# Kernel tuning notes

Measured on AMD Instinct MI355X. Metric: run time of the kernel, lower is better.

Reference implementation:

```python
import jax, jax.numpy as jnp
import numpy as np

D = 512; NH = 8; DH = D // NH; NL = 4; NQ = 4; CB = 1024; DATA = 256
LN_EPS = 1e-5


def _ln(x, s, b):
    m = jnp.mean(x, -1, keepdims=True)
    v = jnp.var(x, -1, keepdims=True)
    return (x - m) / jnp.sqrt(v + LN_EPS) * s + b


def _pos_embed(T, d):
    pos = jnp.arange(T, dtype=jnp.float32)[:, None]
    div = jnp.exp(jnp.arange(0, d, 2, dtype=jnp.float32) * (-np.log(10000.0) / d))
    pe = jnp.zeros((T, d), jnp.float32)
    pe = pe.at[:, 0::2].set(jnp.sin(pos * div))
    pe = pe.at[:, 1::2].set(jnp.cos(pos * div))
    return pe


def _rotate_to(x, q):
    # rotation trick: reflect x through Householder planes so it aligns with q,
    # gradients flow through x only (rotation itself is stop-gradient)
    eps = 1e-6
    nx = jnp.linalg.norm(x, axis=-1, keepdims=True)
    nq = jnp.linalg.norm(q, axis=-1, keepdims=True)
    u = x / jnp.maximum(nx, eps)
    qn = q / jnp.maximum(nq, eps)
    w = u + qn
    w = jax.lax.stop_gradient(w / jnp.maximum(jnp.linalg.norm(w, axis=-1, keepdims=True), eps))
    u_sg = jax.lax.stop_gradient(u)
    qn_sg = jax.lax.stop_gradient(qn)
    out = x - 2.0 * jnp.sum(x * w, -1, keepdims=True) * w \
            + 2.0 * jnp.sum(x * u_sg, -1, keepdims=True) * qn_sg
    return out * jax.lax.stop_gradient(nq / jnp.maximum(nx, eps))


def _vqvae(x, w_in, b_in, qkv_w, qkv_b, out_w, out_b, ln1_s, ln1_b, ln2_s, ln2_b,
           ff1_w, ff1_b, ff2_w, ff2_b, codebooks,
           dec_ln_s, dec_ln_b, dec_w1, dec_b1, dec_w2, dec_b2):
    B, T, _ = x.shape
    h = x @ w_in + b_in + _pos_embed(T, D)[None]
    causal = jnp.triu(jnp.ones((T, T), dtype=bool), k=1)
    scale = 1.0 / np.sqrt(DH)
    for l in range(NL):
        qkv = h @ qkv_w[l] + qkv_b[l]
        q, k, v = jnp.split(qkv, 3, axis=-1)
        q = q.reshape(B, T, NH, DH).transpose(0, 2, 1, 3)
        k = k.reshape(B, T, NH, DH).transpose(0, 2, 1, 3)
        v = v.reshape(B, T, NH, DH).transpose(0, 2, 1, 3)
        scores = jnp.einsum('bhqd,bhkd->bhqk', q, k) * scale
        scores = jnp.where(causal[None, None], -jnp.inf, scores)
        attn = jax.nn.softmax(scores, axis=-1)
        o = jnp.einsum('bhqk,bhkd->bhqd', attn, v).transpose(0, 2, 1, 3).reshape(B, T, D)
        h = _ln(h + o @ out_w[l] + out_b[l], ln1_s[l], ln1_b[l])
        ff = jax.nn.relu(h @ ff1_w[l] + ff1_b[l]) @ ff2_w[l] + ff2_b[l]
        h = _ln(h + ff, ln2_s[l], ln2_b[l])
    # residual VQ with 4 quantizers, rotation trick, commitment loss
    residual = h
    quant_out = jnp.zeros_like(h)
    idx_list, loss_list = [], []
    for qi in range(NQ):
        cb = codebooks[qi]  # [CB, D]
        d = (jnp.sum(residual ** 2, -1, keepdims=True)
             - 2.0 * residual @ cb.T
             + jnp.sum(cb ** 2, -1)[None, None])  # [B,T,CB]
        idx = jnp.argmin(d, axis=-1)
        qv = cb[idx]
        loss_list.append(0.25 * jnp.mean((jax.lax.stop_gradient(qv) - residual) ** 2))
        quant = _rotate_to(residual, qv)
        residual = residual - jax.lax.stop_gradient(quant)
        quant_out = quant_out + quant
        idx_list.append(idx)
    commit = jnp.stack(loss_list)          # [NQ]
    indices = jnp.stack(idx_list, axis=-1)  # [B,T,NQ]
    dh = _ln(quant_out, dec_ln_s, dec_ln_b)
    dec = jax.nn.gelu(dh @ dec_w1 + dec_b1, approximate=False) @ dec_w2 + dec_b2
    return dec, jnp.mean(commit), indices


def setup_inputs() -> dict:
    key = jax.random.key(0)
    ks = jax.random.split(key, 16)
    B, T = 32, 512
    s = 0.02
    return {
        'x': jax.random.normal(ks[0], (B, T, DATA), jnp.float32),
        'w_in': jax.random.normal(ks[1], (DATA, D), jnp.float32) * s,
        'b_in': jnp.zeros((D,), jnp.float32),
        'qkv_w': jax.random.normal(ks[2], (NL, D, 3 * D), jnp.float32) * s,
        'qkv_b': jnp.zeros((NL, 3 * D), jnp.float32),
        'out_w': jax.random.normal(ks[3], (NL, D, D), jnp.float32) * s,
        'out_b': jnp.zeros((NL, D), jnp.float32),
        'ln1_s': jnp.ones((NL, D), jnp.float32),
        'ln1_b': jnp.zeros((NL, D), jnp.float32),
        'ln2_s': jnp.ones((NL, D), jnp.float32),
        'ln2_b': jnp.zeros((NL, D), jnp.float32),
        'ff1_w': jax.random.normal(ks[4], (NL, D, 4 * D), jnp.float32) * s,
        'ff1_b': jnp.zeros((NL, 4 * D), jnp.float32),
        'ff2_w': jax.random.normal(ks[5], (NL, 4 * D, D), jnp.float32) * s,
        'ff2_b': jnp.zeros((NL, D), jnp.float32),
        'codebooks': jax.random.normal(ks[6], (NQ, CB, D), jnp.float32),
        'dec_ln_s': jnp.ones((D,), jnp.float32),
        'dec_ln_b': jnp.zeros((D,), jnp.float32),
        'dec_w1': jax.random.normal(ks[7], (D, D), jnp.float32) * s,
        'dec_b1': jnp.zeros((D,), jnp.float32),
        'dec_w2': jax.random.normal(ks[8], (D, DATA), jnp.float32) * s,
        'dec_b2': jnp.zeros((DATA,), jnp.float32),
    }


def reference(x, w_in, b_in, qkv_w, qkv_b, out_w, out_b, ln1_s, ln1_b, ln2_s, ln2_b,
              ff1_w, ff1_b, ff2_w, ff2_b, codebooks,
              dec_ln_s, dec_ln_b, dec_w1, dec_b1, dec_w2, dec_b2):
    return _vqvae(x, w_in, b_in, qkv_w, qkv_b, out_w, out_b, ln1_s, ln1_b, ln2_s, ln2_b,
                  ff1_w, ff1_b, ff2_w, ff2_b, codebooks,
                  dec_ln_s, dec_ln_b, dec_w1, dec_b1, dec_w2, dec_b2)
```

## Files before the change

kernel.cpp:

```cpp
#include <hip/hip_runtime.h>
#include <hip/hip_bf16.h>
#include <math.h>

#define DD   512
#define NHH  8
#define DHH  64
#define NLL  4
#define NQQ  4
#define CBB  1024
#define DATA 256
#define BB   32
#define TT   512
#define MM   (BB*TT)

typedef __attribute__((ext_vector_type(8))) short bf16x8;
typedef __attribute__((ext_vector_type(4))) float f32x4;

__device__ __forceinline__ float blk_reduce(float v, float* red) {
    const int t = threadIdx.x;
    red[t] = v;
    __syncthreads();
    #pragma unroll
    for (int s = 128; s > 0; s >>= 1) {
        if (t < s) red[t] += red[t + s];
        __syncthreads();
    }
    float r = red[0];
    __syncthreads();
    return r;
}

__device__ __forceinline__ int xcd_remap_lin(int orig, int nwg) {
    int xcd = orig & 7;
    int q = nwg >> 3, r = nwg & 7;
    int base = (xcd < r) ? xcd * (q + 1) : r * (q + 1) + (xcd - r) * q;
    return base + (orig >> 3);
}

__global__ __launch_bounds__(256) void pe_k(float* __restrict__ pe) {
    int t = blockIdx.x;
    int i = threadIdx.x;
    float dv  = expf((float)(2 * i) * -0.017988946039015984f);
    float arg = (float)t * dv;
    pe[(size_t)t * DD + 2 * i]     = sinf(arg);
    pe[(size_t)t * DD + 2 * i + 1] = cosf(arg);
}

__device__ __forceinline__ void cvt3x8(const float* v, bf16x8& q0, bf16x8& q1, bf16x8& q2) {
    #pragma unroll
    for (int j = 0; j < 8; ++j) {
        float f = v[j];
        unsigned short h0 = (unsigned short)((__float_as_uint(f) + 0x8000u) >> 16);
        float f0 = __uint_as_float((unsigned)h0 << 16);
        float r1 = f - f0;
        unsigned short h1 = (unsigned short)((__float_as_uint(r1) + 0x8000u) >> 16);
        float f1 = __uint_as_float((unsigned)h1 << 16);
        float r2 = r1 - f1;
        unsigned short h2 = (unsigned short)((__float_as_uint(r2) + 0x8000u) >> 16);
        q0[j] = (short)h0; q1[j] = (short)h1; q2[j] = (short)h2;
    }
}
__device__ __forceinline__ void cvt3s(float f, short& h0, short& h1, short& h2) {
    unsigned short a0 = (unsigned short)((__float_as_uint(f) + 0x8000u) >> 16);
    float f0 = __uint_as_float((unsigned)a0 << 16);
    float r1 = f - f0;
    unsigned short a1 = (unsigned short)((__float_as_uint(r1) + 0x8000u) >> 16);
    float f1 = __uint_as_float((unsigned)a1 << 16);
    float r2 = r1 - f1;
    unsigned short a2 = (unsigned short)((__float_as_uint(r2) + 0x8000u) >> 16);
    h0 = (short)a0; h1 = (short)a1; h2 = (short)a2;
}

__device__ __forceinline__ void gld_lds16(const short* src, short* lds) {
    __builtin_amdgcn_global_load_lds(
        (const __attribute__((address_space(1))) unsigned int*)src,
        (__attribute__((address_space(3))) unsigned int*)lds,
        16, 0, 0);
}

__global__ __launch_bounds__(256)
void wsplit_tr_k(const float* __restrict__ W, short* __restrict__ P, int N, int K)
{
    const size_t NK = (size_t)N * K;
    const int n = blockIdx.x * 64 + (threadIdx.x & 63);
    #pragma unroll
    for (int it = 0; it < 2; ++it) {
        int k = blockIdx.y * 64 + ((threadIdx.x >> 6) + it * 4) * 8;
        float v[8];
        #pragma unroll
        for (int j = 0; j < 8; ++j) v[j] = W[(size_t)(k + j) * N + n];
        bf16x8 q0, q1, q2;
        cvt3x8(v, q0, q1, q2);
        size_t o = (size_t)n * K + k;
        *(bf16x8*)&P[o] = q0;
        *(bf16x8*)&P[NK + o] = q1;
        *(bf16x8*)&P[2 * NK + o] = q2;
    }
}
__global__ __launch_bounds__(256)
void wsplit_dir_k(const float* __restrict__ W, short* __restrict__ P, int K, size_t NK)
{
    size_t t = (size_t)blockIdx.x * 256 + threadIdx.x;
    size_t n = t >> 6;
    int k = (int)(t & 63) * 8;
    float v[8];
    *(float4*)&v[0] = *(const float4*)(W + n * K + k);
    *(float4*)&v[4] = *(const float4*)(W + n * K + k + 4);
    bf16x8 q0, q1, q2;
    cvt3x8(v, q0, q1, q2);
    size_t o = n * K + k;
    *(bf16x8*)&P[o] = q0;
    *(bf16x8*)&P[NK + o] = q1;
    *(bf16x8*)&P[2 * NK + o] = q2;
}

enum { EPI_BIAS = 0, EPI_RES = 1, EPI_RELU = 2, EPI_GELU = 3, EPI_PE = 4, EPI_PLAIN = 5 };

template<int EPI>
__global__ __launch_bounds__(256, 3)
void mgemm2_k(const float* __restrict__ A, const short* __restrict__ Bp,
              const float* __restrict__ bias, const float* __restrict__ extra,
              float* __restrict__ Cv, int Mdim, int Ndim, int Kdim)
{
    __shared__ short Bs[3 * 128 * 32];
    const size_t NK = (size_t)Ndim * Kdim;
    const int tid = threadIdx.x;
    const int l   = tid & 63;
    const int w   = tid >> 6;

    int lin = xcd_remap_lin(blockIdx.y * gridDim.x + blockIdx.x, gridDim.x * gridDim.y);
    const int bxx = lin % gridDim.x;
    const int byy = lin / gridDim.x;

    const int wm0 = byy * 128 + w * 32;
    const int bn0 = bxx * 128;
    const int lr  = l & 15;
    const int lk  = (l >> 4) * 8;

    int sp[6], sn[6], sk[6];
    #pragma unroll
    for (int i = 0; i < 6; ++i) {
        int f = i * 4096 + tid * 16;
        sp[i] = f >> 13;
        int r = f & 8191;
        sn[i] = r >> 6;
        sk[i] = ((r & 63) >> 1) ^ (((sn[i] >> 1) & 3) << 3);
    }

    f32x4 acc[2][8];
    #pragma unroll
    for (int i = 0; i < 2; ++i)
        #pragma unroll
        for (int j = 0; j < 8; ++j)
            acc[i][j] = (f32x4){0.f, 0.f, 0.f, 0.f};

    for (int k0 = 0; k0 < Kdim; k0 += 32) {
        __syncthreads();
        #pragma unroll
        for (int i = 0; i < 6; ++i) {
            const short* src = Bp + (size_t)sp[i] * NK + (size_t)(bn0 + sn[i]) * Kdim + k0 + sk[i];
            gld_lds16(src, (short*)((char*)Bs + i * 4096 + w * 1024));
        }

        bf16x8 a0[2], a1[2], a2[2];
        #pragma unroll
        for (int mf = 0; mf < 2; ++mf) {
            const float* p = A + (size_t)(wm0 + mf * 16 + lr) * Kdim + k0 + lk;
            float v[8];
            *(float4*)&v[0] = *(const float4*)p;
            *(float4*)&v[4] = *(const float4*)(p + 4);
            cvt3x8(v, a0[mf], a1[mf], a2[mf]);
        }
        __syncthreads();

        #pragma unroll
        for (int nf = 0; nf < 8; ++nf) {
            int brow = nf * 16 + lr;
            int lkx = lk ^ (((brow >> 1) & 3) << 3);
            bf16x8 b0 = *(const bf16x8*)&Bs[0 * 4096 + brow * 32 + lkx];
            bf16x8 b1 = *(const bf16x8*)&Bs[1 * 4096 + brow * 32 + lkx];
            bf16x8 b2 = *(const bf16x8*)&Bs[2 * 4096 + brow * 32 + lkx];
            #pragma unroll
            for (int mf = 0; mf < 2; ++mf) {
                f32x4 c = acc[mf][nf];
                c = __builtin_amdgcn_mfma_f32_16x16x32_bf16(a0[mf], b0, c, 0, 0, 0);
                c = __builtin_amdgcn_mfma_f32_16x16x32_bf16(a0[mf], b1, c, 0, 0, 0);
                c = __builtin_amdgcn_mfma_f32_16x16x32_bf16(a1[mf], b0, c, 0, 0, 0);
                c = __builtin_amdgcn_mfma_f32_16x16x32_bf16(a1[mf], b1, c, 0, 0, 0);
                c = __builtin_amdgcn_mfma_f32_16x16x32_bf16(a0[mf], b2, c, 0, 0, 0);
                c = __builtin_amdgcn_mfma_f32_16x16x32_bf16(a2[mf], b0, c, 0, 0, 0);
                acc[mf][nf] = c;
            }
        }
    }

    #pragma unroll
    for (int mf = 0; mf < 2; ++mf) {
        #pragma unroll
        for (int r = 0; r < 4; ++r) {
            int m = wm0 + mf * 16 + (l >> 4) * 4 + r;
            #pragma unroll
            for (int nf = 0; nf < 8; ++nf) {
                int n = bn0 + nf * 16 + lr;
                float v = acc[mf][nf][r];
                if constexpr (EPI != EPI_PLAIN) v += bias[n];
                if constexpr (EPI == EPI_RES)  v += extra[(size_t)m * Ndim + n];
                if constexpr (EPI == EPI_PE)   v += extra[(size_t)(m & (TT - 1)) * DD + n];
                if constexpr (EPI == EPI_RELU) v = fmaxf(v, 0.0f);
                if constexpr (EPI == EPI_GELU) v = 0.5f * v * (1.0f + erff(v * 0.70710678118654752f));
                Cv[(size_t)m * Ndim + n] = v;
            }
        }
    }
}

__global__ __launch_bounds__(256, 3)
void distmin2_k(const float* __restrict__ A, const short* __restrict__ Bp,
                const float* __restrict__ cn2,
                float* __restrict__ pval, int* __restrict__ pidx)
{
    __shared__ short Bs[3 * 128 * 32];
    const int Ndim = CBB, Kdim = DD;
    const size_t NK = (size_t)Ndim * Kdim;
    const int tid = threadIdx.x;
    const int l   = tid & 63;
    const int w   = tid >> 6;

    int lin = xcd_remap_lin(blockIdx.y * gridDim.x + blockIdx.x, gridDim.x * gridDim.y);
    const int bxx = lin % gridDim.x;
    const int byy = lin / gridDim.x;

    const int wm0 = byy * 128 + w * 32;
    const int bn0 = bxx * 128;
    const int lr  = l & 15;
    const int lk  = (l >> 4) * 8;

    int sp[6], sn[6], sk[6];
    #pragma unroll
    for (int i = 0; i < 6; ++i) {
        int f = i * 4096 + tid * 16;
        sp[i] = f >> 13;
        int r = f & 8191;
        sn[i] = r >> 6;
        sk[i] = ((r & 63) >> 1) ^ (((sn[i] >> 1) & 3) << 3);
    }

    f32x4 acc[2][8];
    #pragma unroll
    for (int i = 0; i < 2; ++i)
        #pragma unroll
        for (int j = 0; j < 8; ++j)
            acc[i][j] = (f32x4){0.f, 0.f, 0.f, 0.f};

    for (int k0 = 0; k0 < Kdim; k0 += 32) {
        __syncthreads();
        #pragma unroll
        for (int i = 0; i < 6; ++i) {
            const short* src = Bp + (size_t)sp[i] * NK + (size_t)(bn0 + sn[i]) * Kdim + k0 + sk[i];
            gld_lds16(src, (short*)((char*)Bs + i * 4096 + w * 1024));
        }

        bf16x8 a0[2], a1[2], a2[2];
        #pragma unroll
        for (int mf = 0; mf < 2; ++mf) {
            const float* p = A + (size_t)(wm0 + mf * 16 + lr) * Kdim + k0 + lk;
            float v[8];
            *(float4*)&v[0] = *(const float4*)p;
            *(float4*)&v[4] = *(const float4*)(p + 4);
            cvt3x8(v, a0[mf], a1[mf], a2[mf]);
        }
        __syncthreads();

        #pragma unroll
        for (int nf = 0; nf < 8; ++nf) {
            int brow = nf * 16 + lr;
            int lkx = lk ^ (((brow >> 1) & 3) << 3);
            bf16x8 b0 = *(const bf16x8*)&Bs[0 * 4096 + brow * 32 + lkx];
            bf16x8 b1 = *(const bf16x8*)&Bs[1 * 4096 + brow * 32 + lkx];
            bf16x8 b2 = *(const bf16x8*)&Bs[2 * 4096 + brow * 32 + lkx];
            #pragma unroll
            for (int mf = 0; mf < 2; ++mf) {
                f32x4 c = acc[mf][nf];
                c = __builtin_amdgcn_mfma_f32_16x16x32_bf16(a0[mf], b0, c, 0, 0, 0);
                c = __builtin_amdgcn_mfma_f32_16x16x32_bf16(a0[mf], b1, c, 0, 0, 0);
                c = __builtin_amdgcn_mfma_f32_16x16x32_bf16(a1[mf], b0, c, 0, 0, 0);
                c = __builtin_amdgcn_mfma_f32_16x16x32_bf16(a1[mf], b1, c, 0, 0, 0);
                c = __builtin_amdgcn_mfma_f32_16x16x32_bf16(a0[mf], b2, c, 0, 0, 0);
                c = __builtin_amdgcn_mfma_f32_16x16x32_bf16(a2[mf], b0, c, 0, 0, 0);
                acc[mf][nf] = c;
            }
        }
    }

    #pragma unroll
    for (int mf = 0; mf < 2; ++mf) {
        #pragma unroll
        for (int r = 0; r < 4; ++r) {
            int m = wm0 + mf * 16 + (l >> 4) * 4 + r;
            float best = INFINITY; int bi = 0x7fffffff;
            #pragma unroll
            for (int nf = 0; nf < 8; ++nf) {
                int n = bn0 + nf * 16 + lr;
                float d = cn2[n] - 2.0f * acc[mf][nf][r];
                if (d < best) { best = d; bi = n; }
            }
            #pragma unroll
            for (int off = 1; off < 16; off <<= 1) {
                float ov = __shfl_xor(best, off);
                int   oi = __shfl_xor(bi, off);
                if (ov < best || (ov == best && oi < bi)) { best = ov; bi = oi; }
            }
            if (lr == 0) {
                pval[(size_t)m * 8 + bxx] = best;
                pidx[(size_t)m * 8 + bxx] = bi;
            }
        }
    }
}

__global__ __launch_bounds__(256)
void argmin8_k(const float* __restrict__ pval, const int* __restrict__ pidx,
               int* __restrict__ idx)
{
    int row = blockIdx.x * 256 + threadIdx.x;
    float best = INFINITY; int bi = 0x7fffffff;
    #pragma unroll
    for (int j = 0; j < 8; ++j) {
        float v = pval[(size_t)row * 8 + j];
        int  ii = pidx[(size_t)row * 8 + j];
        if (v < best || (v == best && ii < bi)) { best = v; bi = ii; }
    }
    idx[row] = bi;
}

__global__ __launch_bounds__(256, 2)
void mattn_k(const float* __restrict__ qkv, float* __restrict__ o)
{
    const int bid = xcd_remap_lin(blockIdx.x, gridDim.x);
    const int qt = bid & 7;
    const int hh = (bid >> 3) & 7;
    const int bb = bid >> 6;
    const int tid = threadIdx.x;
    const int w  = tid >> 6;
    const int l  = tid & 63;
    const int lr = l & 15;
    const int lg = l >> 4;
    const int lk = lg * 8;

    __shared__ short Kb[3][4096];
    __shared__ short Vb[3][4096];
    __shared__ float Ps[4][1024];

    const float* qbase = qkv + (size_t)bb * TT * 1536 + hh * 64;
    const float* kbase = qbase + DD;
    const float* vbase = qbase + 2 * DD;

    bf16x8 qa[2][3];
    {
        int qrow = qt * 64 + w * 16 + lr;
        #pragma unroll
        for (int dc = 0; dc < 2; ++dc) {
            float v[8];
            const float* p = qbase + (size_t)qrow * 1536 + dc * 32 + lk;
            *(float4*)&v[0] = *(const float4*)p;
            *(float4*)&v[4] = *(const float4*)(p + 4);
            cvt3x8(v, qa[dc][0], qa[dc][1], qa[dc][2]);
        }
    }

    f32x4 oacc[4];
    #pragma unroll
    for (int nf = 0; nf < 4; ++nf) oacc[nf] = (f32x4){0.f, 0.f, 0.f, 0.f};
    float m[4], s[4];
    #pragma unroll
    for (int r = 0; r < 4; ++r) { m[r] = -INFINITY; s[r] = 0.f; }

    for (int kt = 0; kt <= qt; ++kt) {
        __syncthreads();
        {
            int kr = tid >> 2, dseg = (tid & 3) * 16;
            const float* p = kbase + (size_t)(kt * 64 + kr) * 1536 + dseg;
            float v[16];
            *(float4*)&v[0]  = *(const float4*)p;
            *(float4*)&v[4]  = *(const float4*)(p + 4);
            *(float4*)&v[8]  = *(const float4*)(p + 8);
            *(float4*)&v[12] = *(const float4*)(p + 12);
            bf16x8 t0, t1, t2, u0, u1, u2;
            cvt3x8(v, t0, t1, t2);
            cvt3x8(v + 8, u0, u1, u2);
            int si = (kr * 64 + dseg) ^ ((kr & 7) << 3);
            *(bf16x8*)&Kb[0][si] = t0; *(bf16x8*)&Kb[0][si ^ 8] = u0;
            *(bf16x8*)&Kb[1][si] = t1; *(bf16x8*)&Kb[1][si ^ 8] = u1;
            *(bf16x8*)&Kb[2][si] = t2; *(bf16x8*)&Kb[2][si ^ 8] = u2;
        }
        {
            int d = tid & 63, kg = (tid >> 6) * 16;
            const float* p = vbase + (size_t)(kt * 64 + kg) * 1536 + d;
            bf16x8 w0[2], w1[2], w2[2];
            #pragma unroll
            for (int i = 0; i < 16; ++i) {
                float f = p[(size_t)i * 1536];
                short h0, h1, h2; cvt3s(f, h0, h1, h2);
                w0[i >> 3][i & 7] = h0; w1[i >> 3][i & 7] = h1; w2[i >> 3][i & 7] = h2;
            }
            int si = (d * 64 + kg) ^ ((d & 7) << 3);
            *(bf16x8*)&Vb[0][si] = w0[0]; *(bf16x8*)&Vb[0][si ^ 8] = w0[1];
            *(bf16x8*)&Vb[1][si] = w1[0]; *(bf16x8*)&Vb[1][si ^ 8] = w1[1];
            *(bf16x8*)&Vb[2][si] = w2[0]; *(bf16x8*)&Vb[2][si ^ 8] = w2[1];
        }
        __syncthreads();

        f32x4 S4[4];
        #pragma unroll
        for (int nf = 0; nf < 4; ++nf) {
            f32x4 acc = (f32x4){0.f, 0.f, 0.f, 0.f};
            int kcol = nf * 16 + lr;
            int rowx = kcol * 64, sw = (kcol & 7) << 3;
            #pragma unroll
            for (int dc = 0; dc < 2; ++dc) {
                int si = rowx + ((dc * 32 + lk) ^ sw);
                bf16x8 b0 = *(const bf16x8*)&Kb[0][si];
                bf16x8 b1 = *(const bf16x8*)&Kb[1][si];
                bf16x8 b2 = *(const bf16x8*)&Kb[2][si];
                acc = __builtin_amdgcn_mfma_f32_16x16x32_bf16(qa[dc][0], b0, acc, 0, 0, 0);
                acc = __builtin_amdgcn_mfma_f32_16x16x32_bf16(qa[dc][0], b1, acc, 0, 0, 0);
                acc = __builtin_amdgcn_mfma_f32_16x16x32_bf16(qa[dc][1], b0, acc, 0, 0, 0);
                acc = __builtin_amdgcn_mfma_f32_16x16x32_bf16(qa[dc][1], b1, acc, 0, 0, 0);
                acc = __builtin_amdgcn_mfma_f32_16x16x32_bf16(qa[dc][0], b2, acc, 0, 0, 0);
                acc = __builtin_amdgcn_mfma_f32_16x16x32_bf16(qa[dc][2], b0, acc, 0, 0, 0);
            }
            S4[nf] = acc;
        }
        #pragma unroll
        for (int nf = 0; nf < 4; ++nf)
            #pragma unroll
            for (int r = 0; r < 4; ++r) S4[nf][r] *= 0.125f;
        if (kt == qt) {
            #pragma unroll
            for (int nf = 0; nf < 4; ++nf) {
                int kg_ = nf * 16 + lr;
                #pragma unroll
                for (int r = 0; r < 4; ++r) {
                    int qg_ = w * 16 + lg * 4 + r;
                    if (kg_ > qg_) S4[nf][r] = -INFINITY;
                }
            }
        }
        float mnew[4], scl[4], psum[4];
        #pragma unroll
        for (int r = 0; r < 4; ++r) {
            float v = fmaxf(fmaxf(S4[0][r], S4[1][r]), fmaxf(S4[2][r], S4[3][r]));
            v = fmaxf(v, __shfl_xor(v, 1));
            v = fmaxf(v, __shfl_xor(v, 2));
            v = fmaxf(v, __shfl_xor(v, 4));
            v = fmaxf(v, __shfl_xor(v, 8));
            mnew[r] = fmaxf(m[r], v);
            scl[r] = expf(m[r] - mnew[r]);
            psum[r] = 0.f;
        }
        #pragma unroll
        for (int nf = 0; nf < 4; ++nf) {
            #pragma unroll
            for (int r = 0; r < 4; ++r) {
                float p = expf(S4[nf][r] - mnew[r]);
                int row = lg * 4 + r;
                int col = nf * 16 + lr;
                Ps[w][row * 64 + (col ^ ((row & 7) << 3))] = p;
                psum[r] += p;
            }
        }
        #pragma unroll
        for (int r = 0; r < 4; ++r) {
            float v = psum[r];
            v += __shfl_xor(v, 1);
            v += __shfl_xor(v, 2);
            v += __shfl_xor(v, 4);
            v += __shfl_xor(v, 8);
            s[r] = s[r] * scl[r] + v;
            m[r] = mnew[r];
        }
        #pragma unroll
        for (int nf = 0; nf < 4; ++nf)
            #pragma unroll
            for (int r = 0; r < 4; ++r) oacc[nf][r] *= scl[r];

        #pragma unroll
        for (int kc = 0; kc < 2; ++kc) {
            int fi = lr * 64 + ((kc * 32 + lk) ^ ((lr & 7) << 3));
            float pv8[8];
            *(float4*)&pv8[0] = *(const float4*)&Ps[w][fi];
            *(float4*)&pv8[4] = *(const float4*)&Ps[w][fi + 4];
            bf16x8 pa0, pa1, pa2;
            cvt3x8(pv8, pa0, pa1, pa2);
            #pragma unroll
            for (int nf = 0; nf < 4; ++nf) {
                int drow = nf * 16 + lr;
                int si = drow * 64 + ((kc * 32 + lk) ^ ((drow & 7) << 3));
                bf16x8 b0 = *(const bf16x8*)&Vb[0][si];
                bf16x8 b1 = *(const bf16x8*)&Vb[1][si];
                bf16x8 b2 = *(const bf16x8*)&Vb[2][si];
                f32x4 c = oacc[nf];
                c = __builtin_amdgcn_mfma_f32_16x16x32_bf16(pa0, b0, c, 0, 0, 0);
                c = __builtin_amdgcn_mfma_f32_16x16x32_bf16(pa0, b1, c, 0, 0, 0);
                c = __builtin_amdgcn_mfma_f32_16x16x32_bf16(pa1, b0, c, 0, 0, 0);
                c = __builtin_amdgcn_mfma_f32_16x16x32_bf16(pa1, b1, c, 0, 0, 0);
                c = __builtin_amdgcn_mfma_f32_16x16x32_bf16(pa0, b2, c, 0, 0, 0);
                c = __builtin_amdgcn_mfma_f32_16x16x32_bf16(pa2, b0, c, 0, 0, 0);
                oacc[nf] = c;
            }
        }
    }

    #pragma unroll
    for (int nf = 0; nf < 4; ++nf) {
        #pragma unroll
        for (int r = 0; r < 4; ++r) {
            int qrow = qt * 64 + w * 16 + lg * 4 + r;
            o[(size_t)(bb * TT + qrow) * DD + hh * 64 + nf * 16 + lr] = oacc[nf][r] / s[r];
        }
    }
}

__global__ __launch_bounds__(256)
void ln_k(const float* __restrict__ src, const float* __restrict__ s,
          const float* __restrict__ b, float* __restrict__ dst)
{
    __shared__ float red[256];
    const int row = blockIdx.x, t = threadIdx.x;
    const size_t base = (size_t)row * DD;
    float x0 = src[base + t], x1 = src[base + 256 + t];
    float mean = blk_reduce(x0 + x1, red) * (1.0f / 512.0f);
    float d0 = x0 - mean, d1 = x1 - mean;
    float var = blk_reduce(d0 * d0 + d1 * d1, red) * (1.0f / 512.0f);
    float inv = 1.0f / sqrtf(var + 1e-5f);
    dst[base + t]       = d0 * inv * s[t] + b[t];
    dst[base + 256 + t] = d1 * inv * s[t + 256] + b[t + 256];
}

__global__ __launch_bounds__(256)
void cn2_k(const float* __restrict__ cb, float* __restrict__ cn2)
{
    __shared__ float red[256];
    const int row = blockIdx.x, t = threadIdx.x;
    float a = cb[(size_t)row * DD + t], b = cb[(size_t)row * DD + 256 + t];
    float tot = blk_reduce(a * a + b * b, red);
    if (t == 0) cn2[row] = tot;
}

__global__ __launch_bounds__(256)
void rotate_k(float* __restrict__ r, const float* __restrict__ cb,
              const int* __restrict__ idx, float* __restrict__ qo,
              float* __restrict__ lp)
{
    __shared__ float red[256];
    const int row = blockIdx.x, t = threadIdx.x;
    const size_t base = (size_t)row * DD;
    const float* qv = cb + (size_t)idx[row] * DD;
    float x0 = r[base + t], x1 = r[base + 256 + t];
    float q0 = qv[t], q1 = qv[t + 256];
    float nx2 = blk_reduce(x0 * x0 + x1 * x1, red);
    float nq2 = blk_reduce(q0 * q0 + q1 * q1, red);
    float dl0 = q0 - x0, dl1 = q1 - x1;
    float ls = blk_reduce(dl0 * dl0 + dl1 * dl1, red);
    if (t == 0) lp[row] = ls;
    const float eps = 1e-6f;
    float nx = sqrtf(nx2), nq = sqrtf(nq2);
    float mx = fmaxf(nx, eps), mq = fmaxf(nq, eps);
    float u0 = x0 / mx, u1 = x1 / mx;
    float qn0 = q0 / mq, qn1 = q1 / mq;
    float w0 = u0 + qn0, w1 = u1 + qn1;
    float nw2 = blk_reduce(w0 * w0 + w1 * w1, red);
    float mw = fmaxf(sqrtf(nw2), eps);
    w0 /= mw; w1 /= mw;
    float xw = blk_reduce(x0 * w0 + x1 * w1, red);
    float xu = blk_reduce(x0 * u0 + x1 * u1, red);
    float scl = nq / mx;
    float o0 = (x0 - 2.0f * xw * w0 + 2.0f * xu * qn0) * scl;
    float o1 = (x1 - 2.0f * xw * w1 + 2.0f * xu * qn1) * scl;
    r[base + t]        = x0 - o0;
    r[base + 256 + t]  = x1 - o1;
    qo[base + t]       += o0;
    qo[base + 256 + t] += o1;
}

__global__ __launch_bounds__(256)
void loss_k(const float* __restrict__ lp, float* __restrict__ out)
{
    __shared__ float red[256];
    const int t = threadIdx.x;
    float cm = 0.f;
    for (int qi = 0; qi < NQQ; ++qi) {
        float s = 0.f;
        for (int i = t; i < MM; i += 256) s += lp[qi * MM + i];
        float tot = blk_reduce(s, red);
        cm += 0.25f * (tot / (float)(MM * DD));
    }
    if (t == 0) out[0] = cm / (float)NQQ;
}

__global__ __launch_bounds__(256)
void idxout_k(const int* __restrict__ idxw, float* __restrict__ out)
{
    int i = blockIdx.x * 256 + threadIdx.x;
    int row = i >> 2, qi = i & 3;
    out[i] = (float)idxw[qi * MM + row];
}

extern "C" void kernel_launch(void* const* d_in, const int* in_sizes, int n_in,
                              void* d_out, int out_size, void* d_ws, size_t ws_size,
                              hipStream_t stream)
{
    const float* x     = (const float*)d_in[0];
    const float* w_in  = (const float*)d_in[1];
    const float* b_in  = (const float*)d_in[2];
    const float* qkv_w = (const float*)d_in[3];
    const float* qkv_b = (const float*)d_in[4];
    const float* out_w = (const float*)d_in[5];
    const float* out_b = (const float*)d_in[6];
    const float* ln1_s = (const float*)d_in[7];
    const float* ln1_b = (const float*)d_in[8];
    const float* ln2_s = (const float*)d_in[9];
    const float* ln2_b = (const float*)d_in[10];
    const float* ff1_w = (const float*)d_in[11];
    const float* ff1_b = (const float*)d_in[12];
    const float* ff2_w = (const float*)d_in[13];
    const float* ff2_b = (const float*)d_in[14];
    const float* cbs   = (const float*)d_in[15];
    const float* dln_s = (const float*)d_in[16];
    const float* dln_b = (const float*)d_in[17];
    const float* dw1   = (const float*)d_in[18];
    const float* db1   = (const float*)d_in[19];
    const float* dw2   = (const float*)d_in[20];
    const float* db2   = (const float*)d_in[21];

    float* ws  = (float*)d_ws;
    float* pe  = ws;
    float* h   = pe + (size_t)262144;
    float* h2  = h + (size_t)MM * DD;
    float* cn2 = h2 + (size_t)MM * DD;
    float* lp  = cn2 + 4096;
    int*   idxw = (int*)(lp + 65536);
    short* wp  = (short*)(idxw + 65536);

    short* p_qkv = wp;
    short* p_out = wp + (size_t)2359296;
    short* p_ff1 = wp + (size_t)3145728;
    short* p_ff2 = wp + (size_t)6291456;
    short* p_win = wp;
    short* p_cb  = wp;
    short* p_dw1 = wp;
    short* p_dw2 = wp + (size_t)786432;
    float* C = (float*)(wp + (size_t)9437184);

    size_t fixed_bytes = (size_t)((char*)C - (char*)ws);
    size_t cbytes = (ws_size > fixed_bytes) ? ws_size - fixed_bytes : 0;
    int CH = 32;
    while (CH > 1 && (size_t)CH * TT * 2048 * sizeof(float) > cbytes) CH >>= 1;
    const int NC = BB / CH;
    const int CR = CH * TT;

    float* qkvc  = C;
    float* attoc = C + (size_t)CR * 1536;
    float* midc  = C;
    float* pval  = C;
    int*   pidx  = (int*)(C + (size_t)CR * 8);
    float* dhc   = C;
    float* dmidc = C + (size_t)CR * DD;

    pe_k<<<dim3(512), dim3(256), 0, stream>>>(pe);
    cn2_k<<<dim3(NQQ * CBB), 256, 0, stream>>>(cbs, cn2);
    wsplit_tr_k<<<dim3(8, 4), 256, 0, stream>>>(w_in, p_win, 512, 256);
    mgemm2_k<EPI_PE><<<dim3(4, 128), 256, 0, stream>>>(x, p_win, b_in, pe, h, MM, DD, 256);

    for (int l = 0; l < NLL; ++l) {
        wsplit_tr_k<<<dim3(24, 8), 256, 0, stream>>>(qkv_w + (size_t)l * DD * 1536, p_qkv, 1536, 512);
        wsplit_tr_k<<<dim3(8, 8), 256, 0, stream>>>(out_w + (size_t)l * DD * DD, p_out, 512, 512);
        wsplit_tr_k<<<dim3(32, 8), 256, 0, stream>>>(ff1_w + (size_t)l * DD * 2048, p_ff1, 2048, 512);
        wsplit_tr_k<<<dim3(8, 32), 256, 0, stream>>>(ff2_w + (size_t)l * 2048 * DD, p_ff2, 512, 2048);
        for (int c = 0; c < NC; ++c) {
            float* hc  = h  + (size_t)c * CR * DD;
            float* h2c = h2 + (size_t)c * CR * DD;
            mgemm2_k<EPI_BIAS><<<dim3(12, CR / 128), 256, 0, stream>>>(
                hc, p_qkv, qkv_b + (size_t)l * 1536, nullptr, qkvc, CR, 1536, DD);
            mattn_k<<<dim3(CH * 64), 256, 0, stream>>>(qkvc, attoc);
            mgemm2_k<EPI_RES><<<dim3(4, CR / 128), 256, 0, stream>>>(
                attoc, p_out, out_b + (size_t)l * DD, hc, h2c, CR, DD, DD);
            ln_k<<<dim3(CR), 256, 0, stream>>>(h2c, ln1_s + (size_t)l * DD, ln1_b + (size_t)l * DD, h2c);
            mgemm2_k<EPI_RELU><<<dim3(16, CR / 128), 256, 0, stream>>>(
                h2c, p_ff1, ff1_b + (size_t)l * 2048, nullptr, midc, CR, 2048, DD);
            mgemm2_k<EPI_RES><<<dim3(4, CR / 128), 256, 0, stream>>>(
                midc, p_ff2, ff2_b + (size_t)l * DD, h2c, hc, CR, DD, 2048);
            ln_k<<<dim3(CR), 256, 0, stream>>>(hc, ln2_s + (size_t)l * DD, ln2_b + (size_t)l * DD, hc);
        }
    }

    hipMemsetAsync(h2, 0, (size_t)MM * DD * sizeof(float), stream);
    for (int qi = 0; qi < NQQ; ++qi) {
        wsplit_dir_k<<<dim3(256), 256, 0, stream>>>(cbs + (size_t)qi * CBB * DD, p_cb, 512, 524288);
        for (int c = 0; c < NC; ++c) {
            float* hc = h + (size_t)c * CR * DD;
            distmin2_k<<<dim3(8, CR / 128), 256, 0, stream>>>(
                hc, p_cb, cn2 + qi * CBB, pval, pidx);
            argmin8_k<<<dim3(CR / 256), 256, 0, stream>>>(pval, pidx,
                                                          idxw + qi * MM + (size_t)c * CR);
        }
        rotate_k<<<dim3(MM), 256, 0, stream>>>(h, cbs + (size_t)qi * CBB * DD,
                                               idxw + qi * MM, h2, lp + qi * MM);
    }

    float* outf = (float*)d_out;
    loss_k<<<dim3(1), 256, 0, stream>>>(lp, outf + (size_t)MM * DATA);
    idxout_k<<<dim3(256), 256, 0, stream>>>(idxw, outf + (size_t)MM * DATA + 1);

    wsplit_tr_k<<<dim3(8, 8), 256, 0, stream>>>(dw1, p_dw1, 512, 512);
    wsplit_tr_k<<<dim3(4, 8), 256, 0, stream>>>(dw2, p_dw2, 256, 512);
    for (int c = 0; c < NC; ++c) {
        float* h2c = h2 + (size_t)c * CR * DD;
        ln_k<<<dim3(CR), 256, 0, stream>>>(h2c, dln_s, dln_b, dhc);
        mgemm2_k<EPI_GELU><<<dim3(4, CR / 128), 256, 0, stream>>>(
            dhc, p_dw1, db1, nullptr, dmidc, CR, DD, DD);
        mgemm2_k<EPI_BIAS><<<dim3(2, CR / 128), 256, 0, stream>>>(
            dmidc, p_dw2, db2, nullptr, outf + (size_t)c * CR * DATA, CR, DATA, DD);
    }
}
```

Measured before the change: 3.565 ms.

## Double-buffer B tiles in LDS for split-bf16 GEMM and distance kernels

Adds a second LDS buffer for the B operand so the async global-to-LDS loads for the next K step are issued before the MFMA work on the current tile. One barrier per iteration replaces two. This aims to hide load latency behind compute. It doubles LDS use per block to 48KB, which may reduce occupancy under the launch_bounds target of 3 blocks. It also relies on the async loads having completed by the time the barrier is reached.

```diff
diff --git a/kernel.cpp b/kernel.cpp
--- a/kernel.cpp
+++ b/kernel.cpp
@@ -122,7 +122,7 @@
               const float* __restrict__ bias, const float* __restrict__ extra,
               float* __restrict__ Cv, int Mdim, int Ndim, int Kdim)
 {
-    __shared__ short Bs[3 * 128 * 32];
+    __shared__ short Bs[2][3 * 4096];
     const size_t NK = (size_t)Ndim * Kdim;
     const int tid = threadIdx.x;
     const int l   = tid & 63;
@@ -154,12 +154,21 @@
         for (int j = 0; j < 8; ++j)
             acc[i][j] = (f32x4){0.f, 0.f, 0.f, 0.f};
 
+    #pragma unroll
+    for (int i = 0; i < 6; ++i) {
+        const short* src = Bp + (size_t)sp[i] * NK + (size_t)(bn0 + sn[i]) * Kdim + sk[i];
+        gld_lds16(src, (short*)((char*)&Bs[0][0] + i * 4096 + w * 1024));
+    }
+    __syncthreads();
+
+    int cur = 0;
     for (int k0 = 0; k0 < Kdim; k0 += 32) {
-        __syncthreads();
-        #pragma unroll
-        for (int i = 0; i < 6; ++i) {
-            const short* src = Bp + (size_t)sp[i] * NK + (size_t)(bn0 + sn[i]) * Kdim + k0 + sk[i];
-            gld_lds16(src, (short*)((char*)Bs + i * 4096 + w * 1024));
+        if (k0 + 32 < Kdim) {
+            #pragma unroll
+            for (int i = 0; i < 6; ++i) {
+                const short* src = Bp + (size_t)sp[i] * NK + (size_t)(bn0 + sn[i]) * Kdim + (k0 + 32) + sk[i];
+                gld_lds16(src, (short*)((char*)&Bs[cur ^ 1][0] + i * 4096 + w * 1024));
+            }
         }
 
         bf16x8 a0[2], a1[2], a2[2];
@@ -171,15 +180,15 @@
             *(float4*)&v[4] = *(const float4*)(p + 4);
             cvt3x8(v, a0[mf], a1[mf], a2[mf]);
         }
-        __syncthreads();
-
+
+        const short* Bh = &Bs[cur][0];
         #pragma unroll
         for (int nf = 0; nf < 8; ++nf) {
             int brow = nf * 16 + lr;
             int lkx = lk ^ (((brow >> 1) & 3) << 3);
-            bf16x8 b0 = *(const bf16x8*)&Bs[0 * 4096 + brow * 32 + lkx];
-            bf16x8 b1 = *(const bf16x8*)&Bs[1 * 4096 + brow * 32 + lkx];
-            bf16x8 b2 = *(const bf16x8*)&Bs[2 * 4096 + brow * 32 + lkx];
+            bf16x8 b0 = *(const bf16x8*)&Bh[0 * 4096 + brow * 32 + lkx];
+            bf16x8 b1 = *(const bf16x8*)&Bh[1 * 4096 + brow * 32 + lkx];
+            bf16x8 b2 = *(const bf16x8*)&Bh[2 * 4096 + brow * 32 + lkx];
             #pragma unroll
             for (int mf = 0; mf < 2; ++mf) {
                 f32x4 c = acc[mf][nf];
@@ -192,6 +201,8 @@
                 acc[mf][nf] = c;
             }
         }
+        __syncthreads();
+        cur ^= 1;
     }
 
     #pragma unroll
@@ -219,7 +230,7 @@
                 const float* __restrict__ cn2,
                 float* __restrict__ pval, int* __restrict__ pidx)
 {
-    __shared__ short Bs[3 * 128 * 32];
+    __shared__ short Bs[2][3 * 4096];
     const int Ndim = CBB, Kdim = DD;
     const size_t NK = (size_t)Ndim * Kdim;
     const int tid = threadIdx.x;
@@ -252,12 +263,21 @@
         for (int j = 0; j < 8; ++j)
             acc[i][j] = (f32x4){0.f, 0.f, 0.f, 0.f};
 
+    #pragma unroll
+    for (int i = 0; i < 6; ++i) {
+        const short* src = Bp + (size_t)sp[i] * NK + (size_t)(bn0 + sn[i]) * Kdim + sk[i];
+        gld_lds16(src, (short*)((char*)&Bs[0][0] + i * 4096 + w * 1024));
+    }
+    __syncthreads();
+
+    int cur = 0;
     for (int k0 = 0; k0 < Kdim; k0 += 32) {
-        __syncthreads();
-        #pragma unroll
-        for (int i = 0; i < 6; ++i) {
-            const short* src = Bp + (size_t)sp[i] * NK + (size_t)(bn0 + sn[i]) * Kdim + k0 + sk[i];
-            gld_lds16(src, (short*)((char*)Bs + i * 4096 + w * 1024));
+        if (k0 + 32 < Kdim) {
+            #pragma unroll
+            for (int i = 0; i < 6; ++i) {
+                const short* src = Bp + (size_t)sp[i] * NK + (size_t)(bn0 + sn[i]) * Kdim + (k0 + 32) + sk[i];
+                gld_lds16(src, (short*)((char*)&Bs[cur ^ 1][0] + i * 4096 + w * 1024));
+            }
         }
 
         bf16x8 a0[2], a1[2], a2[2];
@@ -269,15 +289,15 @@
             *(float4*)&v[4] = *(const float4*)(p + 4);
             cvt3x8(v, a0[mf], a1[mf], a2[mf]);
         }
-        __syncthreads();
-
+
+        const short* Bh = &Bs[cur][0];
         #pragma unroll
         for (int nf = 0; nf < 8; ++nf) {
             int brow = nf * 16 + lr;
             int lkx = lk ^ (((brow >> 1) & 3) << 3);
-            bf16x8 b0 = *(const bf16x8*)&Bs[0 * 4096 + brow * 32 + lkx];
-            bf16x8 b1 = *(const bf16x8*)&Bs[1 * 4096 + brow * 32 + lkx];
-            bf16x8 b2 = *(const bf16x8*)&Bs[2 * 4096 + brow * 32 + lkx];
+            bf16x8 b0 = *(const bf16x8*)&Bh[0 * 4096 + brow * 32 + lkx];
+            bf16x8 b1 = *(const bf16x8*)&Bh[1 * 4096 + brow * 32 + lkx];
+            bf16x8 b2 = *(const bf16x8*)&Bh[2 * 4096 + brow * 32 + lkx];
             #pragma unroll
             for (int mf = 0; mf < 2; ++mf) {
                 f32x4 c = acc[mf][nf];
@@ -290,6 +310,8 @@
                 acc[mf][nf] = c;
             }
         }
+        __syncthreads();
+        cur ^= 1;
     }
 
     #pragma unroll
```

Result: no change. 3.499 ms (-1.8%).
